# Optimization experiments

Measured on AMD Instinct MI355X. Metric: run time of the kernel, lower is better.

Reference implementation:

```python
import jax, jax.numpy as jnp
import numpy as np

EPS = 1e-5
H = 8
N_BUCKETS = 32


def _instance_norm(x, gamma, beta):
    # x: [B, N, D]; torch InstanceNorm1d normalizes over the N (length) dim
    # per channel per batch element, using biased variance.
    m = jnp.mean(x, axis=1, keepdims=True)
    v = jnp.var(x, axis=1, keepdims=True)
    return (x - m) * jax.lax.rsqrt(v + EPS) * gamma + beta


def setup_inputs() -> dict:
    key = jax.random.key(0)
    ks = jax.random.split(key, 12)
    B, N, D, d_ff = 4, 512, 128, 512
    s = 1.0 / np.sqrt(D)
    sf = 1.0 / np.sqrt(d_ff)
    u = lambda k, shape, lim: jax.random.uniform(k, shape, jnp.float32, -lim, lim)
    return {
        "h": jax.random.normal(ks[0], (B, N, D), jnp.float32),
        "coords": jax.random.uniform(ks[1], (B, N, 2), jnp.float32),
        "W_Q": u(ks[2], (D, D), s),
        "W_K": u(ks[3], (D, D), s),
        "W_V": u(ks[4], (D, D), s),
        "W_O": u(ks[5], (D, D), s),
        "emb": jax.random.normal(ks[6], (N_BUCKETS, D), jnp.float32),  # n_heads*d_k == D
        "ffn_w1": u(ks[7], (D, d_ff), s),
        "ffn_b1": u(ks[8], (d_ff,), s),
        "ffn_w2": u(ks[9], (d_ff, D), sf),
        "ffn_b2": u(ks[10], (D,), sf),
        "gamma1": jnp.ones((D,), jnp.float32),
        "beta1": jnp.zeros((D,), jnp.float32),
        "gamma2": jnp.ones((D,), jnp.float32),
        "beta2": jnp.zeros((D,), jnp.float32),
    }


def reference(h, coords, W_Q, W_K, W_V, W_O, emb, ffn_w1, ffn_b1, ffn_w2,
              ffn_b2, gamma1, beta1, gamma2, beta2):
    B, N, D = h.shape
    Dk = D // H
    Q = (h @ W_Q).reshape(B, N, H, Dk)
    K = (h @ W_K).reshape(B, N, H, Dk)
    V = (h @ W_V).reshape(B, N, H, Dk)
    # content scores: [B, H, N, N]
    scores = jnp.einsum('bnhd,bmhd->bhnm', Q, K) / np.sqrt(Dk)
    # relative-distance bucket embeddings for all (i, j) pairs
    diff = coords[:, :, None, :] - coords[:, None, :, :]          # [B,N,N,2]
    dist = jax.lax.stop_gradient(jnp.sqrt(jnp.sum(diff * diff, -1)))
    buckets = jnp.clip((dist * N_BUCKETS).astype(jnp.int32), 0, N_BUCKETS - 1)
    r = emb[buckets].reshape(B, N, N, H, Dk)                      # [B,N,N,H,Dk]
    scores = scores + jnp.einsum('bnhd,bnmhd->bhnm', Q, r)
    attn = jax.nn.softmax(scores, axis=-1)
    h_attn = jnp.einsum('bhnm,bmhd->bnhd', attn, V).reshape(B, N, D) @ W_O
    h1 = _instance_norm(h + h_attn, gamma1, beta1)
    h_ffn = jax.nn.relu(h1 @ ffn_w1 + ffn_b1) @ ffn_w2 + ffn_b2
    return _instance_norm(h1 + h_ffn, gamma2, beta2)
```

## Files before the change

kernel.cpp:

```cpp
#include <hip/hip_runtime.h>
#include <hip/hip_bf16.h>

#define B_  4
#define N_  512
#define D_  128
#define H_  8
#define DK  16
#define DFF 512
#define NB  32
#define KS  8

template <int NT, int K, int ROWS, int RELU>
__global__ __launch_bounds__(256) void gemv_kernel(
    const float* __restrict__ A,
    const float* __restrict__ B0, const float* __restrict__ B1, const float* __restrict__ B2,
    float* __restrict__ C0, float* __restrict__ C1, float* __restrict__ C2,
    const float* __restrict__ bias, const float* __restrict__ resid)
{
    const float* Bw = blockIdx.z == 0 ? B0 : (blockIdx.z == 1 ? B1 : B2);
    float*       C  = blockIdx.z == 0 ? C0 : (blockIdx.z == 1 ? C1 : C2);
    const int wave = threadIdx.x >> 6;
    const int lane = threadIdx.x & 63;
    const int rbase = __builtin_amdgcn_readfirstlane((blockIdx.x * 4 + wave) * ROWS);
    const int col = blockIdx.y * 128 + lane * 2;

    float acc[ROWS][2] = {};

#pragma unroll 2
    for (int k0 = 0; k0 < K; k0 += 4) {
        float4 a4[ROWS];
#pragma unroll
        for (int j = 0; j < ROWS; ++j)
            a4[j] = *(const float4*)&A[(size_t)(rbase + j) * K + k0];
#pragma unroll
        for (int kk = 0; kk < 4; ++kk) {
            float2 bv = *(const float2*)&Bw[(size_t)(k0 + kk) * NT + col];
#pragma unroll
            for (int j = 0; j < ROWS; ++j) {
                float a = (&a4[j].x)[kk];
                acc[j][0] += a * bv.x;
                acc[j][1] += a * bv.y;
            }
        }
    }

    float2 bb = make_float2(0.f, 0.f);
    if (bias) bb = *(const float2*)&bias[col];
#pragma unroll
    for (int j = 0; j < ROWS; ++j) {
        const int row = rbase + j;
        float o0 = acc[j][0] + bb.x;
        float o1 = acc[j][1] + bb.y;
        if (resid) {
            float2 rv = *(const float2*)&resid[(size_t)row * NT + col];
            o0 += rv.x; o1 += rv.y;
        }
        if (RELU) { o0 = fmaxf(o0, 0.f); o1 = fmaxf(o1, 0.f); }
        *(float2*)&C[(size_t)row * NT + col] = make_float2(o0, o1);
    }
}

__global__ __launch_bounds__(256) void qe_kernel(const float* __restrict__ Q,
                                                 const float* __restrict__ emb,
                                                 float* __restrict__ QE)
{
    int idx = blockIdx.x * 256 + threadIdx.x;
    int k   = idx & (NB - 1);
    int hh  = (idx >> 5) & (H_ - 1);
    int row = idx >> 8;
    const float4* qp = (const float4*)(Q + (size_t)row * D_ + hh * DK);
    const float4* ep = (const float4*)(emb + (size_t)k * D_ + hh * DK);
    float4 q0 = qp[0], q1 = qp[1], q2 = qp[2], q3 = qp[3];
    float4 e0 = ep[0], e1 = ep[1], e2 = ep[2], e3 = ep[3];
    float dot = q0.x*e0.x + q0.y*e0.y + q0.z*e0.z + q0.w*e0.w
              + q1.x*e1.x + q1.y*e1.y + q1.z*e1.z + q1.w*e1.w
              + q2.x*e2.x + q2.y*e2.y + q2.z*e2.z + q2.w*e2.w
              + q3.x*e3.x + q3.y*e3.y + q3.z*e3.z + q3.w*e3.w;
    QE[idx] = dot;
}

__global__ __launch_bounds__(256) void attn5_kernel(
    const float* __restrict__ Q, const float* __restrict__ K, const float* __restrict__ V,
    const float* __restrict__ QE, const float* __restrict__ coords,
    float* __restrict__ P)
{
    const int tid  = threadIdx.x;
    const int wave = tid >> 6;
    const int lane = tid & 63;
    const int bid  = blockIdx.x;
    const int ks    = bid & 7;
    const int chunk = (bid >> 3) & 7;
    const int h     = (bid >> 6) & (H_ - 1);
    const int b     = bid >> 9;

    const int n   = chunk * 64 + lane;
    const int row = b * N_ + n;

    __shared__ float qel[64][NB + 1];
    __shared__ float ckrd[64][2];
    __shared__ float accl[4][64][17];

    {
        int r = tid >> 2, part = tid & 3;
        const float* src = QE + ((size_t)(b * N_ + chunk * 64 + r) * H_ + h) * NB + part * 8;
#pragma unroll
        for (int j = 0; j < 8; ++j) qel[r][part * 8 + j] = src[j];
    }
    if (tid < 128)
        ((float*)ckrd)[tid] = coords[(size_t)(b * N_ + ks * 64) * 2 + tid];

    const float4* qp = (const float4*)(Q + (size_t)row * D_ + h * DK);
    const float4 q0 = qp[0], q1 = qp[1], q2 = qp[2], q3 = qp[3];
    const float cx = coords[(size_t)row * 2 + 0];
    const float cy = coords[(size_t)row * 2 + 1];

    __syncthreads();

    const size_t hdbase = (size_t)b * N_ * D_ + h * DK;

    float l = 0.f;
    float acc[16] = {};

    const int m0 = __builtin_amdgcn_readfirstlane(ks * 64 + wave * 16);
#pragma unroll 4
    for (int i = 0; i < 16; ++i) {
        const int m = m0 + i;
        const float4* kp = (const float4*)(K + hdbase + (size_t)m * D_);
        const float4 k0 = kp[0], k1 = kp[1], k2 = kp[2], k3 = kp[3];
        float dot = q0.x*k0.x + q0.y*k0.y + q0.z*k0.z + q0.w*k0.w
                  + q1.x*k1.x + q1.y*k1.y + q1.z*k1.z + q1.w*k1.w
                  + q2.x*k2.x + q2.y*k2.y + q2.z*k2.z + q2.w*k2.w
                  + q3.x*k3.x + q3.y*k3.y + q3.z*k3.z + q3.w*k3.w;
        const int mloc = m - ks * 64;
        float dx = cx - ckrd[mloc][0], dy = cy - ckrd[mloc][1];
        float dist = sqrtf(dx * dx + dy * dy);
        int bucket = (int)(dist * 32.0f);
        bucket = bucket > (NB - 1) ? (NB - 1) : bucket;
        float s = dot * 0.25f + qel[lane][bucket];
        float p = __expf(s);
        l += p;
        const float4* vp = (const float4*)(V + hdbase + (size_t)m * D_);
        const float4 v0 = vp[0], v1 = vp[1], v2 = vp[2], v3 = vp[3];
        acc[0]  += p * v0.x; acc[1]  += p * v0.y; acc[2]  += p * v0.z; acc[3]  += p * v0.w;
        acc[4]  += p * v1.x; acc[5]  += p * v1.y; acc[6]  += p * v1.z; acc[7]  += p * v1.w;
        acc[8]  += p * v2.x; acc[9]  += p * v2.y; acc[10] += p * v2.z; acc[11] += p * v2.w;
        acc[12] += p * v3.x; acc[13] += p * v3.y; acc[14] += p * v3.z; acc[15] += p * v3.w;
    }

    accl[wave][lane][16] = l;
#pragma unroll
    for (int j = 0; j < 16; ++j) accl[wave][lane][j] = acc[j];
    __syncthreads();

    float* pb = P + (size_t)bid * (64 * 17);
    for (int i = tid; i < 64 * 17; i += 256) {
        int r = i / 17, j = i - r * 17;
        pb[i] = accl[0][r][j] + accl[1][r][j] + accl[2][r][j] + accl[3][r][j];
    }
}

__global__ __launch_bounds__(256) void attn_combine_kernel(
    const float* __restrict__ P, float* __restrict__ AO)
{
    int idx = blockIdx.x * 256 + threadIdx.x;
    int d  = idx & (D_ - 1);
    int r  = idx >> 7;
    int h  = d >> 4, dk = d & 15;
    int b  = r >> 9, n = r & (N_ - 1);
    int chunk = n >> 6, rl = n & 63;
    size_t base = ((size_t)(((b * H_ + h) * 8 + chunk) * KS)) * (64 * 17) + (size_t)rl * 17;
    float a = 0.f, l = 0.f;
#pragma unroll
    for (int s = 0; s < KS; ++s) {
        const float* ps = P + base + (size_t)s * (64 * 17);
        a += ps[dk];
        l += ps[16];
    }
    AO[idx] = a / l;
}

__global__ __launch_bounds__(256) void stats_kernel(const float* __restrict__ X,
    const float* __restrict__ gamma, const float* __restrict__ beta,
    float* __restrict__ T1, float* __restrict__ T2)
{
    const int b  = blockIdx.x >> 3;
    const int dg = blockIdx.x & 7;
    const int dl = threadIdx.x & 15;
    const int nc = threadIdx.x >> 4;
    const int d  = dg * 16 + dl;
    const float* xb = X + (size_t)b * N_ * D_ + d;
    float s = 0.f, q = 0.f;
    for (int i = 0; i < 32; ++i) {
        float x = xb[(size_t)(nc * 32 + i) * D_];
        s += x; q += x * x;
    }
    __shared__ float ls[16][17], lq[16][17];
    ls[nc][dl] = s; lq[nc][dl] = q;
    __syncthreads();
    if (threadIdx.x < 16) {
        float S = 0.f, Q2 = 0.f;
#pragma unroll
        for (int i = 0; i < 16; ++i) { S += ls[i][threadIdx.x]; Q2 += lq[i][threadIdx.x]; }
        int dd = dg * 16 + threadIdx.x;
        float mean = S * (1.0f / N_);
        float var  = Q2 * (1.0f / N_) - mean * mean;
        float r = 1.0f / sqrtf(var + 1e-5f);
        float t1 = r * gamma[dd];
        T1[b * D_ + dd] = t1;
        T2[b * D_ + dd] = beta[dd] - mean * t1;
    }
}

__global__ __launch_bounds__(256) void apply_kernel(const float* __restrict__ X,
    const float* __restrict__ T1, const float* __restrict__ T2, float* __restrict__ Y)
{
    int idx = (blockIdx.x * 256 + threadIdx.x) * 4;
    int d = idx & (D_ - 1);
    int b = idx >> 16;
    float4 x  = *(const float4*)&X[idx];
    float4 t1 = *(const float4*)&T1[b * D_ + d];
    float4 t2 = *(const float4*)&T2[b * D_ + d];
    float4 y;
    y.x = x.x * t1.x + t2.x; y.y = x.y * t1.y + t2.y;
    y.z = x.z * t1.z + t2.z; y.w = x.w * t1.w + t2.w;
    *(float4*)&Y[idx] = y;
}

__global__ __launch_bounds__(256) void ffn2s_kernel(
    const float* __restrict__ F1, const float* __restrict__ w2, float* __restrict__ Pf)
{
    const int wave = threadIdx.x >> 6;
    const int lane = threadIdx.x & 63;
    const int rbase = __builtin_amdgcn_readfirstlane((blockIdx.x * 4 + wave) * 8);
    const int col = lane * 2;
    const int s = blockIdx.z;
    const int kbeg = s * 128;

    float acc[8][2] = {};
#pragma unroll 2
    for (int k0 = kbeg; k0 < kbeg + 128; k0 += 4) {
        float4 a4[8];
#pragma unroll
        for (int j = 0; j < 8; ++j)
            a4[j] = *(const float4*)&F1[(size_t)(rbase + j) * DFF + k0];
#pragma unroll
        for (int kk = 0; kk < 4; ++kk) {
            float2 bv = *(const float2*)&w2[(size_t)(k0 + kk) * D_ + col];
#pragma unroll
            for (int j = 0; j < 8; ++j) {
                float a = (&a4[j].x)[kk];
                acc[j][0] += a * bv.x;
                acc[j][1] += a * bv.y;
            }
        }
    }
#pragma unroll
    for (int j = 0; j < 8; ++j)
        *(float2*)&Pf[((size_t)s * (B_ * N_) + rbase + j) * D_ + col] =
            make_float2(acc[j][0], acc[j][1]);
}

__global__ __launch_bounds__(256) void fcomb_kernel(
    const float* __restrict__ Pf, const float* __restrict__ b2,
    const float* __restrict__ H1, float* __restrict__ X2)
{
    int idx = (blockIdx.x * 256 + threadIdx.x) * 4;
    int d = idx & (D_ - 1);
    float4 o = *(const float4*)&b2[d];
    float4 r = *(const float4*)&H1[idx];
    o.x += r.x; o.y += r.y; o.z += r.z; o.w += r.w;
#pragma unroll
    for (int s = 0; s < 4; ++s) {
        float4 p = *(const float4*)&Pf[(size_t)s * (B_ * N_ * D_) + idx];
        o.x += p.x; o.y += p.y; o.z += p.z; o.w += p.w;
    }
    *(float4*)&X2[idx] = o;
}

extern "C" void kernel_launch(void* const* d_in, const int* in_sizes, int n_in,
                              void* d_out, int out_size, void* d_ws, size_t ws_size,
                              hipStream_t stream)
{
    const float* h      = (const float*)d_in[0];
    const float* coords = (const float*)d_in[1];
    const float* W_Q    = (const float*)d_in[2];
    const float* W_K    = (const float*)d_in[3];
    const float* W_V    = (const float*)d_in[4];
    const float* W_O    = (const float*)d_in[5];
    const float* emb    = (const float*)d_in[6];
    const float* w1     = (const float*)d_in[7];
    const float* b1     = (const float*)d_in[8];
    const float* w2     = (const float*)d_in[9];
    const float* b2     = (const float*)d_in[10];
    const float* g1     = (const float*)d_in[11];
    const float* be1    = (const float*)d_in[12];
    const float* g2     = (const float*)d_in[13];
    const float* be2    = (const float*)d_in[14];
    float* out = (float*)d_out;

    float* ws = (float*)d_ws;
    const size_t R = (size_t)B_ * N_;
    float* Qb  = ws;
    float* Kb  = Qb + R * D_;
    float* Vb  = Kb + R * D_;
    float* QEb = Vb + R * D_;
    float* AO  = QEb + R * H_ * NB;
    float* X1  = AO + R * D_;
    float* H1  = X1 + R * D_;
    float* F1  = H1 + R * D_;
    float* X2  = F1 + R * DFF;
    float* Pb  = X2 + R * D_;
    float* Pf  = Pb + (size_t)2048 * 64 * 17;
    float* T1a = Pf + (size_t)4 * R * D_;
    float* T2a = T1a + B_ * D_;
    float* T1b = T2a + B_ * D_;
    float* T2b = T1b + B_ * D_;

    gemv_kernel<128, 128, 4, 0><<<dim3(128, 1, 3), 256, 0, stream>>>(
        h, W_Q, W_K, W_V, Qb, Kb, Vb, nullptr, nullptr);
    qe_kernel<<<dim3(2048), 256, 0, stream>>>(Qb, emb, QEb);
    attn5_kernel<<<dim3(2048), 256, 0, stream>>>(Qb, Kb, Vb, QEb, coords, Pb);
    attn_combine_kernel<<<dim3((int)(R * D_) / 256), 256, 0, stream>>>(Pb, AO);
    gemv_kernel<128, 128, 4, 0><<<dim3(128, 1, 1), 256, 0, stream>>>(
        AO, W_O, W_O, W_O, X1, X1, X1, nullptr, h);
    stats_kernel<<<dim3(B_ * 8), 256, 0, stream>>>(X1, g1, be1, T1a, T2a);
    apply_kernel<<<dim3((int)(R * D_) / 1024), 256, 0, stream>>>(X1, T1a, T2a, H1);
    gemv_kernel<512, 128, 8, 1><<<dim3(64, 4, 1), 256, 0, stream>>>(
        H1, w1, w1, w1, F1, F1, F1, b1, nullptr);
    ffn2s_kernel<<<dim3(64, 1, 4), 256, 0, stream>>>(F1, w2, Pf);
    fcomb_kernel<<<dim3((int)(R * D_) / 1024), 256, 0, stream>>>(Pf, b2, H1, X2);
    stats_kernel<<<dim3(B_ * 8), 256, 0, stream>>>(X2, g2, be2, T1b, T2b);
    apply_kernel<<<dim3((int)(R * D_) / 1024), 256, 0, stream>>>(X2, T1b, T2b, out);
}
```

Baseline: 91.30 us.

## Fuse QKV with QE, combine with O-proj, norm-apply into FFN1, stats with apply

Cuts the pipeline from twelve launches to seven. The QE dot products move into the Q projection blocks, and the split-K attention combine is fused into the output projection through LDS. The first instance-norm apply is folded into the FFN1 A-tile load and into the residual add, and the final stats and apply are merged into one kernel. FFN2 split-K grows from 4 to 8. This removes launch overhead and several full-tensor round trips through memory. In exchange, the fused stats/apply runs on only 32 blocks, and the larger split-K doubles partial-sum traffic.

```diff
diff --git a/kernel.cpp b/kernel.cpp
--- a/kernel.cpp
+++ b/kernel.cpp
@@ -9,74 +9,68 @@
 #define DFF 512
 #define NB  32
 #define KS  8
-
-template <int NT, int K, int ROWS, int RELU>
-__global__ __launch_bounds__(256) void gemv_kernel(
+#define FS  8
+
+__global__ __launch_bounds__(256) void qkv_qe_kernel(
     const float* __restrict__ A,
-    const float* __restrict__ B0, const float* __restrict__ B1, const float* __restrict__ B2,
-    float* __restrict__ C0, float* __restrict__ C1, float* __restrict__ C2,
-    const float* __restrict__ bias, const float* __restrict__ resid)
-{
-    const float* Bw = blockIdx.z == 0 ? B0 : (blockIdx.z == 1 ? B1 : B2);
-    float*       C  = blockIdx.z == 0 ? C0 : (blockIdx.z == 1 ? C1 : C2);
+    const float* __restrict__ WQ, const float* __restrict__ WK, const float* __restrict__ WV,
+    const float* __restrict__ emb,
+    float* __restrict__ Qo, float* __restrict__ Ko, float* __restrict__ Vo,
+    float* __restrict__ QE)
+{
+    const float* Bw = blockIdx.z == 0 ? WQ : (blockIdx.z == 1 ? WK : WV);
+    float*       C  = blockIdx.z == 0 ? Qo : (blockIdx.z == 1 ? Ko : Vo);
     const int wave = threadIdx.x >> 6;
     const int lane = threadIdx.x & 63;
-    const int rbase = __builtin_amdgcn_readfirstlane((blockIdx.x * 4 + wave) * ROWS);
-    const int col = blockIdx.y * 128 + lane * 2;
-
-    float acc[ROWS][2] = {};
-
+    const int rbase = __builtin_amdgcn_readfirstlane((blockIdx.x * 4 + wave) * 4);
+    const int col = lane * 2;
+
+    float acc[4][2] = {};
 #pragma unroll 2
-    for (int k0 = 0; k0 < K; k0 += 4) {
-        float4 a4[ROWS];
-#pragma unroll
-        for (int j = 0; j < ROWS; ++j)
-            a4[j] = *(const float4*)&A[(size_t)(rbase + j) * K + k0];
+    for (int k0 = 0; k0 < D_; k0 += 4) {
+        float4 a4[4];
+#pragma unroll
+        for (int j = 0; j < 4; ++j)
+            a4[j] = *(const float4*)&A[(size_t)(rbase + j) * D_ + k0];
 #pragma unroll
         for (int kk = 0; kk < 4; ++kk) {
-            float2 bv = *(const float2*)&Bw[(size_t)(k0 + kk) * NT + col];
-#pragma unroll
-            for (int j = 0; j < ROWS; ++j) {
+            float2 bv = *(const float2*)&Bw[(size_t)(k0 + kk) * D_ + col];
+#pragma unroll
+            for (int j = 0; j < 4; ++j) {
                 float a = (&a4[j].x)[kk];
                 acc[j][0] += a * bv.x;
                 acc[j][1] += a * bv.y;
             }
         }
     }
-
-    float2 bb = make_float2(0.f, 0.f);
-    if (bias) bb = *(const float2*)&bias[col];
-#pragma unroll
-    for (int j = 0; j < ROWS; ++j) {
-        const int row = rbase + j;
-        float o0 = acc[j][0] + bb.x;
-        float o1 = acc[j][1] + bb.y;
-        if (resid) {
-            float2 rv = *(const float2*)&resid[(size_t)row * NT + col];
-            o0 += rv.x; o1 += rv.y;
+#pragma unroll
+    for (int j = 0; j < 4; ++j)
+        *(float2*)&C[(size_t)(rbase + j) * D_ + col] = make_float2(acc[j][0], acc[j][1]);
+
+    if (blockIdx.z == 0) {
+        __shared__ float Qls[16][132];
+#pragma unroll
+        for (int j = 0; j < 4; ++j)
+            *(float2*)&Qls[wave * 4 + j][col] = make_float2(acc[j][0], acc[j][1]);
+        __syncthreads();
+        const int r  = threadIdx.x >> 4;
+        const int hh = (threadIdx.x & 15) >> 1;
+        const int k0 = (threadIdx.x & 1) * 16;
+        const int grow = blockIdx.x * 16 + r;
+        const float4* qv = (const float4*)&Qls[r][hh * DK];
+        const float4 qa = qv[0], qb = qv[1], qc = qv[2], qd = qv[3];
+        float* qe_out = QE + ((size_t)grow * H_ + hh) * NB + k0;
+#pragma unroll 4
+        for (int k = 0; k < 16; ++k) {
+            const float4* ep = (const float4*)(emb + (size_t)(k0 + k) * D_ + hh * DK);
+            float4 e0 = ep[0], e1 = ep[1], e2 = ep[2], e3 = ep[3];
+            float dot = qa.x*e0.x + qa.y*e0.y + qa.z*e0.z + qa.w*e0.w
+                      + qb.x*e1.x + qb.y*e1.y + qb.z*e1.z + qb.w*e1.w
+                      + qc.x*e2.x + qc.y*e2.y + qc.z*e2.z + qc.w*e2.w
+                      + qd.x*e3.x + qd.y*e3.y + qd.z*e3.z + qd.w*e3.w;
+            qe_out[k] = dot;
         }
-        if (RELU) { o0 = fmaxf(o0, 0.f); o1 = fmaxf(o1, 0.f); }
-        *(float2*)&C[(size_t)row * NT + col] = make_float2(o0, o1);
-    }
-}
-
-__global__ __launch_bounds__(256) void qe_kernel(const float* __restrict__ Q,
-                                                 const float* __restrict__ emb,
-                                                 float* __restrict__ QE)
-{
-    int idx = blockIdx.x * 256 + threadIdx.x;
-    int k   = idx & (NB - 1);
-    int hh  = (idx >> 5) & (H_ - 1);
-    int row = idx >> 8;
-    const float4* qp = (const float4*)(Q + (size_t)row * D_ + hh * DK);
-    const float4* ep = (const float4*)(emb + (size_t)k * D_ + hh * DK);
-    float4 q0 = qp[0], q1 = qp[1], q2 = qp[2], q3 = qp[3];
-    float4 e0 = ep[0], e1 = ep[1], e2 = ep[2], e3 = ep[3];
-    float dot = q0.x*e0.x + q0.y*e0.y + q0.z*e0.z + q0.w*e0.w
-              + q1.x*e1.x + q1.y*e1.y + q1.z*e1.z + q1.w*e1.w
-              + q2.x*e2.x + q2.y*e2.y + q2.z*e2.z + q2.w*e2.w
-              + q3.x*e3.x + q3.y*e3.y + q3.z*e3.z + q3.w*e3.w;
-    QE[idx] = dot;
+    }
 }
 
 __global__ __launch_bounds__(256) void attn5_kernel(
@@ -159,24 +153,80 @@
     }
 }
 
-__global__ __launch_bounds__(256) void attn_combine_kernel(
-    const float* __restrict__ P, float* __restrict__ AO)
-{
-    int idx = blockIdx.x * 256 + threadIdx.x;
-    int d  = idx & (D_ - 1);
-    int r  = idx >> 7;
-    int h  = d >> 4, dk = d & 15;
-    int b  = r >> 9, n = r & (N_ - 1);
-    int chunk = n >> 6, rl = n & 63;
-    size_t base = ((size_t)(((b * H_ + h) * 8 + chunk) * KS)) * (64 * 17) + (size_t)rl * 17;
-    float a = 0.f, l = 0.f;
-#pragma unroll
-    for (int s = 0; s < KS; ++s) {
-        const float* ps = P + base + (size_t)s * (64 * 17);
-        a += ps[dk];
-        l += ps[16];
-    }
-    AO[idx] = a / l;
+__global__ __launch_bounds__(256) void oproj_kernel(
+    const float* __restrict__ P, const float* __restrict__ WO,
+    const float* __restrict__ hres, float* __restrict__ X1)
+{
+    const int tid = threadIdx.x;
+    const int gr0 = blockIdx.x * 16;
+    __shared__ float AOls[16][128];
+    __shared__ float lsl[16][8];
+
+    if (tid < 128) {
+        int r = tid >> 3, hh = tid & 7;
+        int gr = gr0 + r;
+        int b = gr >> 9, n = gr & (N_ - 1);
+        int chunk = n >> 6, rl = n & 63;
+        size_t base = ((size_t)(((b * H_ + hh) * 8 + chunk) * KS)) * (64 * 17) + (size_t)rl * 17;
+        float l = 0.f;
+#pragma unroll
+        for (int s = 0; s < KS; ++s) l += P[base + (size_t)s * (64 * 17) + 16];
+        lsl[r][hh] = l;
+    }
+
+    float asum[8];
+#pragma unroll
+    for (int j = 0; j < 8; ++j) {
+        int i = tid + j * 256;
+        int r = i >> 7, d = i & 127;
+        int gr = gr0 + r;
+        int b = gr >> 9, n = gr & (N_ - 1);
+        int chunk = n >> 6, rl = n & 63;
+        int hh = d >> 4, dk = d & 15;
+        size_t base = ((size_t)(((b * H_ + hh) * 8 + chunk) * KS)) * (64 * 17) + (size_t)rl * 17 + dk;
+        float a = 0.f;
+#pragma unroll
+        for (int s = 0; s < KS; ++s) a += P[base + (size_t)s * (64 * 17)];
+        asum[j] = a;
+    }
+    __syncthreads();
+#pragma unroll
+    for (int j = 0; j < 8; ++j) {
+        int i = tid + j * 256;
+        int r = i >> 7, d = i & 127;
+        AOls[r][d] = asum[j] / lsl[r][d >> 4];
+    }
+    __syncthreads();
+
+    const int wave = tid >> 6;
+    const int lane = tid & 63;
+    const int rl = wave * 4;
+    const int grb = __builtin_amdgcn_readfirstlane(gr0 + rl);
+    const int col = lane * 2;
+
+    float acc[4][2] = {};
+#pragma unroll 2
+    for (int k0 = 0; k0 < D_; k0 += 4) {
+        float4 a4[4];
+#pragma unroll
+        for (int j = 0; j < 4; ++j) a4[j] = *(const float4*)&AOls[rl + j][k0];
+#pragma unroll
+        for (int kk = 0; kk < 4; ++kk) {
+            float2 bv = *(const float2*)&WO[(size_t)(k0 + kk) * D_ + col];
+#pragma unroll
+            for (int j = 0; j < 4; ++j) {
+                float a = (&a4[j].x)[kk];
+                acc[j][0] += a * bv.x;
+                acc[j][1] += a * bv.y;
+            }
+        }
+    }
+#pragma unroll
+    for (int j = 0; j < 4; ++j) {
+        float2 rv = *(const float2*)&hres[(size_t)(grb + j) * D_ + col];
+        *(float2*)&X1[(size_t)(grb + j) * D_ + col] =
+            make_float2(acc[j][0] + rv.x, acc[j][1] + rv.y);
+    }
 }
 
 __global__ __launch_bounds__(256) void stats_kernel(const float* __restrict__ X,
@@ -211,41 +261,40 @@
     }
 }
 
-__global__ __launch_bounds__(256) void apply_kernel(const float* __restrict__ X,
-    const float* __restrict__ T1, const float* __restrict__ T2, float* __restrict__ Y)
-{
-    int idx = (blockIdx.x * 256 + threadIdx.x) * 4;
-    int d = idx & (D_ - 1);
-    int b = idx >> 16;
-    float4 x  = *(const float4*)&X[idx];
-    float4 t1 = *(const float4*)&T1[b * D_ + d];
-    float4 t2 = *(const float4*)&T2[b * D_ + d];
-    float4 y;
-    y.x = x.x * t1.x + t2.x; y.y = x.y * t1.y + t2.y;
-    y.z = x.z * t1.z + t2.z; y.w = x.w * t1.w + t2.w;
-    *(float4*)&Y[idx] = y;
-}
-
-__global__ __launch_bounds__(256) void ffn2s_kernel(
-    const float* __restrict__ F1, const float* __restrict__ w2, float* __restrict__ Pf)
-{
+__global__ __launch_bounds__(256) void ffn1_kernel(
+    const float* __restrict__ X1, const float* __restrict__ T1, const float* __restrict__ T2,
+    const float* __restrict__ w1, const float* __restrict__ b1, float* __restrict__ F1)
+{
+    __shared__ float Als[32][128];
+    const int gr0 = blockIdx.x * 32;
+    const int b = gr0 >> 9;
+    for (int i = threadIdx.x * 4; i < 32 * 128; i += 1024) {
+        int r = i >> 7, c = i & 127;
+        float4 x  = *(const float4*)&X1[(size_t)(gr0 + r) * D_ + c];
+        float4 t1 = *(const float4*)&T1[b * D_ + c];
+        float4 t2 = *(const float4*)&T2[b * D_ + c];
+        float4 y;
+        y.x = x.x * t1.x + t2.x; y.y = x.y * t1.y + t2.y;
+        y.z = x.z * t1.z + t2.z; y.w = x.w * t1.w + t2.w;
+        *(float4*)&Als[r][c] = y;
+    }
+    __syncthreads();
+
     const int wave = threadIdx.x >> 6;
     const int lane = threadIdx.x & 63;
-    const int rbase = __builtin_amdgcn_readfirstlane((blockIdx.x * 4 + wave) * 8);
-    const int col = lane * 2;
-    const int s = blockIdx.z;
-    const int kbeg = s * 128;
+    const int rl = wave * 8;
+    const int grb = __builtin_amdgcn_readfirstlane(gr0 + rl);
+    const int col = blockIdx.y * 128 + lane * 2;
 
     float acc[8][2] = {};
 #pragma unroll 2
-    for (int k0 = kbeg; k0 < kbeg + 128; k0 += 4) {
+    for (int k0 = 0; k0 < D_; k0 += 4) {
         float4 a4[8];
 #pragma unroll
-        for (int j = 0; j < 8; ++j)
-            a4[j] = *(const float4*)&F1[(size_t)(rbase + j) * DFF + k0];
+        for (int j = 0; j < 8; ++j) a4[j] = *(const float4*)&Als[rl + j][k0];
 #pragma unroll
         for (int kk = 0; kk < 4; ++kk) {
-            float2 bv = *(const float2*)&w2[(size_t)(k0 + kk) * D_ + col];
+            float2 bv = *(const float2*)&w1[(size_t)(k0 + kk) * DFF + col];
 #pragma unroll
             for (int j = 0; j < 8; ++j) {
                 float a = (&a4[j].x)[kk];
@@ -254,6 +303,43 @@
             }
         }
     }
+    float2 bb = *(const float2*)&b1[col];
+#pragma unroll
+    for (int j = 0; j < 8; ++j) {
+        float o0 = fmaxf(acc[j][0] + bb.x, 0.f);
+        float o1 = fmaxf(acc[j][1] + bb.y, 0.f);
+        *(float2*)&F1[(size_t)(grb + j) * DFF + col] = make_float2(o0, o1);
+    }
+}
+
+__global__ __launch_bounds__(256) void ffn2s_kernel(
+    const float* __restrict__ F1, const float* __restrict__ w2, float* __restrict__ Pf)
+{
+    const int wave = threadIdx.x >> 6;
+    const int lane = threadIdx.x & 63;
+    const int rbase = __builtin_amdgcn_readfirstlane((blockIdx.x * 4 + wave) * 8);
+    const int col = lane * 2;
+    const int s = blockIdx.z;
+    const int kbeg = s * (DFF / FS);
+
+    float acc[8][2] = {};
+#pragma unroll 2
+    for (int k0 = kbeg; k0 < kbeg + DFF / FS; k0 += 4) {
+        float4 a4[8];
+#pragma unroll
+        for (int j = 0; j < 8; ++j)
+            a4[j] = *(const float4*)&F1[(size_t)(rbase + j) * DFF + k0];
+#pragma unroll
+        for (int kk = 0; kk < 4; ++kk) {
+            float2 bv = *(const float2*)&w2[(size_t)(k0 + kk) * D_ + col];
+#pragma unroll
+            for (int j = 0; j < 8; ++j) {
+                float a = (&a4[j].x)[kk];
+                acc[j][0] += a * bv.x;
+                acc[j][1] += a * bv.y;
+            }
+        }
+    }
 #pragma unroll
     for (int j = 0; j < 8; ++j)
         *(float2*)&Pf[((size_t)s * (B_ * N_) + rbase + j) * D_ + col] =
@@ -262,19 +348,66 @@
 
 __global__ __launch_bounds__(256) void fcomb_kernel(
     const float* __restrict__ Pf, const float* __restrict__ b2,
-    const float* __restrict__ H1, float* __restrict__ X2)
+    const float* __restrict__ X1, const float* __restrict__ T1, const float* __restrict__ T2,
+    float* __restrict__ X2)
 {
     int idx = (blockIdx.x * 256 + threadIdx.x) * 4;
     int d = idx & (D_ - 1);
-    float4 o = *(const float4*)&b2[d];
-    float4 r = *(const float4*)&H1[idx];
-    o.x += r.x; o.y += r.y; o.z += r.z; o.w += r.w;
-#pragma unroll
-    for (int s = 0; s < 4; ++s) {
+    int b = idx >> 16;
+    float4 o  = *(const float4*)&b2[d];
+    float4 x1 = *(const float4*)&X1[idx];
+    float4 t1 = *(const float4*)&T1[b * D_ + d];
+    float4 t2 = *(const float4*)&T2[b * D_ + d];
+    o.x += x1.x * t1.x + t2.x; o.y += x1.y * t1.y + t2.y;
+    o.z += x1.z * t1.z + t2.z; o.w += x1.w * t1.w + t2.w;
+#pragma unroll
+    for (int s = 0; s < FS; ++s) {
         float4 p = *(const float4*)&Pf[(size_t)s * (B_ * N_ * D_) + idx];
         o.x += p.x; o.y += p.y; o.z += p.z; o.w += p.w;
     }
     *(float4*)&X2[idx] = o;
+}
+
+__global__ __launch_bounds__(256) void stats_apply_kernel(const float* __restrict__ X,
+    const float* __restrict__ gamma, const float* __restrict__ beta,
+    float* __restrict__ Y)
+{
+    const int b  = blockIdx.x >> 3;
+    const int dg = blockIdx.x & 7;
+    const int dl = threadIdx.x & 15;
+    const int nc = threadIdx.x >> 4;
+    const int d  = dg * 16 + dl;
+    const float* xb = X + (size_t)b * N_ * D_ + d;
+    float s = 0.f, q = 0.f;
+#pragma unroll 4
+    for (int i = 0; i < 32; ++i) {
+        float x = xb[(size_t)(nc * 32 + i) * D_];
+        s += x; q += x * x;
+    }
+    __shared__ float ls[16][17], lq[16][17];
+    __shared__ float t1l[16], t2l[16];
+    ls[nc][dl] = s; lq[nc][dl] = q;
+    __syncthreads();
+    if (threadIdx.x < 16) {
+        float S = 0.f, Q2 = 0.f;
+#pragma unroll
+        for (int i = 0; i < 16; ++i) { S += ls[i][threadIdx.x]; Q2 += lq[i][threadIdx.x]; }
+        int dd = dg * 16 + threadIdx.x;
+        float mean = S * (1.0f / N_);
+        float var  = Q2 * (1.0f / N_) - mean * mean;
+        float r = 1.0f / sqrtf(var + 1e-5f);
+        float t1 = r * gamma[dd];
+        t1l[threadIdx.x] = t1;
+        t2l[threadIdx.x] = beta[dd] - mean * t1;
+    }
+    __syncthreads();
+    const float t1 = t1l[dl], t2 = t2l[dl];
+    float* yb = Y + (size_t)b * N_ * D_ + d;
+#pragma unroll 4
+    for (int i = 0; i < 32; ++i) {
+        size_t off = (size_t)(nc * 32 + i) * D_;
+        yb[off] = xb[off] * t1 + t2;
+    }
 }
 
 extern "C" void kernel_launch(void* const* d_in, const int* in_sizes, int n_in,
@@ -304,31 +437,21 @@
     float* Kb  = Qb + R * D_;
     float* Vb  = Kb + R * D_;
     float* QEb = Vb + R * D_;
-    float* AO  = QEb + R * H_ * NB;
-    float* X1  = AO + R * D_;
-    float* H1  = X1 + R * D_;
-    float* F1  = H1 + R * D_;
+    float* X1  = QEb + R * H_ * NB;
+    float* F1  = X1 + R * D_;
     float* X2  = F1 + R * DFF;
     float* Pb  = X2 + R * D_;
     float* Pf  = Pb + (size_t)2048 * 64 * 17;
-    float* T1a = Pf + (size_t)4 * R * D_;
+    float* T1a = Pf + (size_t)FS * R * D_;
     float* T2a = T1a + B_ * D_;
-    float* T1b = T2a + B_ * D_;
-    float* T2b = T1b + B_ * D_;
-
-    gemv_kernel<128, 128, 4, 0><<<dim3(128, 1, 3), 256, 0, stream>>>(
-        h, W_Q, W_K, W_V, Qb, Kb, Vb, nullptr, nullptr);
-    qe_kernel<<<dim3(2048), 256, 0, stream>>>(Qb, emb, QEb);
+
+    qkv_qe_kernel<<<dim3(128, 1, 3), 256, 0, stream>>>(
+        h, W_Q, W_K, W_V, emb, Qb, Kb, Vb, QEb);
     attn5_kernel<<<dim3(2048), 256, 0, stream>>>(Qb, Kb, Vb, QEb, coords, Pb);
-    attn_combine_kernel<<<dim3((int)(R * D_) / 256), 256, 0, stream>>>(Pb, AO);
-    gemv_kernel<128, 128, 4, 0><<<dim3(128, 1, 1), 256, 0, stream>>>(
-        AO, W_O, W_O, W_O, X1, X1, X1, nullptr, h);
+    oproj_kernel<<<dim3((int)R / 16), 256, 0, stream>>>(Pb, W_O, h, X1);
     stats_kernel<<<dim3(B_ * 8), 256, 0, stream>>>(X1, g1, be1, T1a, T2a);
-    apply_kernel<<<dim3((int)(R * D_) / 1024), 256, 0, stream>>>(X1, T1a, T2a, H1);
-    gemv_kernel<512, 128, 8, 1><<<dim3(64, 4, 1), 256, 0, stream>>>(
-        H1, w1, w1, w1, F1, F1, F1, b1, nullptr);
-    ffn2s_kernel<<<dim3(64, 1, 4), 256, 0, stream>>>(F1, w2, Pf);
-    fcomb_kernel<<<dim3((int)(R * D_) / 1024), 256, 0, stream>>>(Pf, b2, H1, X2);
-    stats_kernel<<<dim3(B_ * 8), 256, 0, stream>>>(X2, g2, be2, T1b, T2b);
-    apply_kernel<<<dim3((int)(R * D_) / 1024), 256, 0, stream>>>(X2, T1b, T2b, out);
-}
+    ffn1_kernel<<<dim3(64, 4), 256, 0, stream>>>(X1, T1a, T2a, w1, b1, F1);
+    ffn2s_kernel<<<dim3(64, 1, FS), 256, 0, stream>>>(F1, w2, Pf);
+    fcomb_kernel<<<dim3((int)(R * D_) / 1024), 256, 0, stream>>>(Pf, b2, X1, T1a, T2a, X2);
+    stats_apply_kernel<<<dim3(B_ * 8), 256, 0, stream>>>(X2, g2, be2, out);
+}
```

Measured after the change: 86.62 us. 1.05x faster.
